# Performance work log

Measured on AMD Instinct MI355X. Metric: run time of the kernel, lower is better.

Reference implementation:

```python
import jax, jax.numpy as jnp
import numpy as np

ALPHA = 0.2  # LeakyReLU negative slope (pyGAT default)
NEG_INF = -9e15


def setup_inputs() -> dict:
    key = jax.random.key(0)
    ks = jax.random.split(key, 8)
    N, IN, OUT, H, C = 4096, 512, 64, 8, 10
    x = jax.random.normal(ks[0], (N, IN), dtype=jnp.float32)
    adj = jax.random.randint(ks[1], (N, N), 0, 2, dtype=jnp.int32)
    W = jax.random.normal(ks[2], (H, IN, OUT), dtype=jnp.float32) * 0.05
    a1 = jax.random.normal(ks[3], (H, OUT), dtype=jnp.float32) * 0.05
    a2 = jax.random.normal(ks[4], (H, OUT), dtype=jnp.float32) * 0.05
    Wo = jax.random.normal(ks[5], (H * OUT, C), dtype=jnp.float32) * 0.05
    ao1 = jax.random.normal(ks[6], (C,), dtype=jnp.float32) * 0.05
    ao2 = jax.random.normal(ks[7], (C,), dtype=jnp.float32) * 0.05
    return {"x": x, "adj": adj, "W": W, "a1": a1, "a2": a2,
            "Wo": Wo, "ao1": ao1, "ao2": ao2}


def _multi_head_gat(h, mask, W, a1, a2):
    # h: [N, F_in], W: [H, F_in, F_out], a1/a2: [H, F_out], mask: [N, N] bool
    Wh = jnp.einsum('ni,hio->hno', h, W)            # [H, N, F_out]
    f1 = jnp.einsum('hno,ho->hn', Wh, a1)           # [H, N]
    f2 = jnp.einsum('hno,ho->hn', Wh, a2)           # [H, N]
    e = f1[:, :, None] + f2[:, None, :]             # [H, N, N]
    e = jnp.where(e > 0, e, ALPHA * e)              # LeakyReLU(0.2)
    e = jnp.where(mask[None, :, :], e, NEG_INF)     # adjacency mask
    attn = jax.nn.softmax(e, axis=-1)               # [H, N, N]
    return jnp.einsum('hnm,hmo->hno', attn, Wh)     # [H, N, F_out]


def reference(x, adj, W, a1, a2, Wo, ao1, ao2):
    mask = adj > 0
    # hidden heads (concat=True -> ELU on concatenated output)
    heads = _multi_head_gat(x, mask, W, a1, a2)          # [H, N, O]
    H, N, O = heads.shape
    hcat = jnp.transpose(heads, (1, 0, 2)).reshape(N, H * O)
    hcat = jax.nn.elu(hcat)
    # output layer (concat=False -> no ELU)
    out = _multi_head_gat(hcat, mask, Wo[None], ao1[None], ao2[None])[0]  # [N, C]
    return jax.nn.log_softmax(out, axis=-1)
```

## Files before the change

### kernel.cpp

```cpp
#include <hip/hip_runtime.h>
#include <hip/hip_bf16.h>
#include <hip/hip_fp16.h>

typedef __bf16 bf16x8 __attribute__((ext_vector_type(8)));
typedef _Float16 h8_t __attribute__((ext_vector_type(8)));
typedef _Float16 v2h __attribute__((ext_vector_type(2)));
typedef short short8 __attribute__((ext_vector_type(8)));
typedef float f32x4 __attribute__((ext_vector_type(4)));

union BF8 { short8 s; bf16x8 b; };
union H8  { short8 s; h8_t h; unsigned w[4]; };
union HU  { _Float16 f; unsigned short u; };

#define N_NODES 4096
#define F_IN 512
#define F_OUT 64
#define NHEAD 8
#define HID 512
#define NCLS 10
#define GAT_ALPHA 0.2f
#define MSPLIT 4
#define WST 4096
#define NWORD (N_NODES / 64)
#define RB 32
#define CB 64
#define NIT ((N_NODES / MSPLIT) / CB)
#define RB2 16
#define MS2 8
#define MT2 (N_NODES / MS2 / 64)

#if defined(__has_builtin)
#if __has_builtin(__builtin_amdgcn_fdot2)
#define FDOT2(a, b, c) __builtin_amdgcn_fdot2((a), (b), (c), false)
#endif
#endif
#ifndef FDOT2
#define FDOT2(a, b, c) ((c) + (float)(a)[0] * (float)(b)[0] + (float)(a)[1] * (float)(b)[1])
#endif

__device__ inline unsigned short f2bf(float f) {
  unsigned u = __builtin_bit_cast(unsigned, f);
  unsigned r = (u + 0x7FFFu + ((u >> 16) & 1u)) >> 16;
  return (unsigned short)r;
}
__device__ inline float bf2f(unsigned short h) {
  unsigned u = ((unsigned)h) << 16;
  return __builtin_bit_cast(float, u);
}

__global__ __launch_bounds__(256) void pack_adj_kernel(
    const int* __restrict__ adj, unsigned long long* __restrict__ bits) {
  int wid = blockIdx.x * 4 + (threadIdx.x >> 6);
  int l = threadIdx.x & 63;
  unsigned long long m = __ballot(adj[(size_t)wid * 64 + l] != 0);
  if (l == 0) bits[wid] = m;
}

__global__ __launch_bounds__(256) void gemm1_kernel(
    const float* __restrict__ x, const float* __restrict__ W,
    const float* __restrict__ a1, const float* __restrict__ a2,
    unsigned short* __restrict__ WhbT, float* __restrict__ rho1,
    unsigned short* __restrict__ E2f16, unsigned short* __restrict__ E2sf16) {
  __shared__ short As[64 * 40];
  __shared__ short Bs[64 * 40];
  __shared__ short Ts[64 * 72];
  const int bx = blockIdx.x;
  const int h  = blockIdx.y;
  const int t  = threadIdx.x;
  const int w  = t >> 6, l = t & 63;
  const int lr = l & 15, ls = l >> 4;
  f32x4 acc[4] = {};
  for (int k0 = 0; k0 < F_IN; k0 += 32) {
    {
      int r = t >> 2, c0 = (t & 3) * 8;
      const float* src = x + (bx * 64 + r) * F_IN + k0 + c0;
      float4 v0 = *(const float4*)src;
      float4 v1 = *(const float4*)(src + 4);
      short8 sv;
      sv[0]=f2bf(v0.x); sv[1]=f2bf(v0.y); sv[2]=f2bf(v0.z); sv[3]=f2bf(v0.w);
      sv[4]=f2bf(v1.x); sv[5]=f2bf(v1.y); sv[6]=f2bf(v1.z); sv[7]=f2bf(v1.w);
      *(short8*)&As[r * 40 + c0] = sv;
    }
    {
      int kk = t >> 3, o0 = (t & 7) * 8;
      const float* src = W + ((h * F_IN) + k0 + kk) * F_OUT + o0;
      float4 v0 = *(const float4*)src;
      float4 v1 = *(const float4*)(src + 4);
      float vv[8] = {v0.x, v0.y, v0.z, v0.w, v1.x, v1.y, v1.z, v1.w};
      #pragma unroll
      for (int i = 0; i < 8; ++i) Bs[(o0 + i) * 40 + kk] = f2bf(vv[i]);
    }
    __syncthreads();
    BF8 a; a.s = *(short8*)&As[(w * 16 + lr) * 40 + ls * 8];
    #pragma unroll
    for (int fc = 0; fc < 4; ++fc) {
      BF8 b; b.s = *(short8*)&Bs[(fc * 16 + lr) * 40 + ls * 8];
      acc[fc] = __builtin_amdgcn_mfma_f32_16x16x32_bf16(a.b, b.b, acc[fc], 0, 0, 0);
    }
    __syncthreads();
  }
  #pragma unroll
  for (int fc = 0; fc < 4; ++fc)
    #pragma unroll
    for (int j = 0; j < 4; ++j) {
      HU hu; hu.f = (_Float16)acc[fc][j];
      Ts[(fc * 16 + lr) * 72 + (w * 16 + ls * 4 + j)] = (short)hu.u;
    }
  __syncthreads();
  {
    int col = t >> 2, seg = t & 3;
    short8 o0 = *(short8*)&Ts[col * 72 + seg * 16];
    short8 o1 = *(short8*)&Ts[col * 72 + seg * 16 + 8];
    unsigned short* dst = WhbT + (size_t)(h * F_OUT + col) * WST + bx * 64 + seg * 16;
    *(short8*)dst = o0;
    *(short8*)(dst + 8) = o1;
  }
  float a1c[4], a2c[4];
  #pragma unroll
  for (int fc = 0; fc < 4; ++fc) {
    a1c[fc] = a1[h * F_OUT + fc * 16 + lr];
    a2c[fc] = a2[h * F_OUT + fc * 16 + lr];
  }
  #pragma unroll
  for (int j = 0; j < 4; ++j) {
    float s1 = 0.f, s2 = 0.f;
    #pragma unroll
    for (int fc = 0; fc < 4; ++fc) { s1 += acc[fc][j] * a1c[fc]; s2 += acc[fc][j] * a2c[fc]; }
    #pragma unroll
    for (int off = 1; off <= 8; off <<= 1) {
      s1 += __shfl_xor(s1, off, 64);
      s2 += __shfl_xor(s2, off, 64);
    }
    if (lr == 0) {
      int row = bx * 64 + w * 16 + ls * 4 + j;
      int idx = h * N_NODES + row;
      rho1[idx] = __expf((GAT_ALPHA - 1.f) * s1);
      HU u1; u1.f = (_Float16)__expf(s2);
      HU u2; u2.f = (_Float16)__expf(GAT_ALPHA * s2);
      E2f16[idx]  = u1.u;
      E2sf16[idx] = u2.u;
    }
  }
}

__global__ __launch_bounds__(512, 4) void att1_kernel(
    const unsigned long long* __restrict__ adjbits,
    const float* __restrict__ rho1,
    const unsigned short* __restrict__ E2f16, const unsigned short* __restrict__ E2sf16,
    const unsigned short* __restrict__ WhbT,
    float* __restrict__ accP, float* __restrict__ SP) {
  __shared__ __align__(16) short Bt[NHEAD][64 * CB];
  const int nb = blockIdx.x * RB;
  const int q  = blockIdx.y;
  const int t  = threadIdx.x;
  const int h  = t >> 6;
  const int l  = t & 63;
  const int r  = l & 15, s = l >> 4;

  const float rho0  = rho1[h * N_NODES + nb + r];
  const float rho1v = rho1[h * N_NODES + nb + 16 + r];
  const v2h rh0 = {(_Float16)rho0, (_Float16)rho0};
  const v2h rh1 = {(_Float16)rho1v, (_Float16)rho1v};
  const v2h ones = {(_Float16)1.0f, (_Float16)1.0f};
  const unsigned short* __restrict__ E2h  = E2f16  + h * N_NODES;
  const unsigned short* __restrict__ E2sh = E2sf16 + h * N_NODES;
  const unsigned long long* __restrict__ ab0 = adjbits + (size_t)(nb + r) * NWORD;
  const unsigned long long* __restrict__ ab1 = adjbits + (size_t)(nb + 16 + r) * NWORD;

  const unsigned short* gsrc0 =
      WhbT + (size_t)(h * F_OUT + (l >> 3)) * WST + (((l & 7) ^ (l >> 3)) * 8);

  const int tb0 = q * (N_NODES / MSPLIT);

  #pragma unroll
  for (int i = 0; i < 8; ++i)
    __builtin_amdgcn_global_load_lds(
        (const __attribute__((address_space(1))) void*)(gsrc0 + tb0 + (size_t)(i * 8) * WST),
        (__attribute__((address_space(3))) void*)&Bt[h][i * 512], 16, 0, 0);

  float S0 = 0.f, S1 = 0.f;
  f32x4 acc[2][4] = {};
  for (int it = 0; it < NIT; ++it) {
    const int tb = tb0 + it * CB;
    const unsigned long long mk0 = ab0[tb >> 6];
    const unsigned long long mk1 = ab1[tb >> 6];
    H8 a0[2], a1f[2];
    #pragma unroll
    for (int kf = 0; kf < 2; ++kf) {
      const int cb = tb + kf * 32 + s * 8;
      uint4 ew = *(const uint4*)(E2h + cb);
      uint4 sw = *(const uint4*)(E2sh + cb);
      const unsigned ewa[4] = {ew.x, ew.y, ew.z, ew.w};
      const unsigned swa[4] = {sw.x, sw.y, sw.z, sw.w};
      const unsigned bm0 = (unsigned)(mk0 >> (kf * 32 + s * 8)) & 0xffu;
      const unsigned bm1 = (unsigned)(mk1 >> (kf * 32 + s * 8)) & 0xffu;
      #pragma unroll
      for (int p = 0; p < 4; ++p) {
        const v2h e2 = __builtin_bit_cast(v2h, ewa[p]);
        const v2h es = __builtin_bit_cast(v2h, swa[p]);
        const unsigned lo0 = ((bm0 >> (2 * p)) & 1u) ? 0x0000FFFFu : 0u;
        const unsigned hi0 = ((bm0 >> (2 * p + 1)) & 1u) ? 0xFFFF0000u : 0u;
        unsigned q0w = __builtin_bit_cast(unsigned, __builtin_elementwise_max(e2, (v2h)(rh0 * es))) & (lo0 | hi0);
        S0 = FDOT2(__builtin_bit_cast(v2h, q0w), ones, S0);
        a0[kf].w[p] = q0w;
        const unsigned lo1 = ((bm1 >> (2 * p)) & 1u) ? 0x0000FFFFu : 0u;
        const unsigned hi1 = ((bm1 >> (2 * p + 1)) & 1u) ? 0xFFFF0000u : 0u;
        unsigned q1w = __builtin_bit_cast(unsigned, __builtin_elementwise_max(e2, (v2h)(rh1 * es))) & (lo1 | hi1);
        S1 = FDOT2(__builtin_bit_cast(v2h, q1w), ones, S1);
        a1f[kf].w[p] = q1w;
      }
    }
    asm volatile("s_waitcnt vmcnt(0)" ::: "memory");
    H8 b[2][4];
    #pragma unroll
    for (int kf = 0; kf < 2; ++kf)
      #pragma unroll
      for (int fc = 0; fc < 4; ++fc)
        b[kf][fc].s = *(short8*)&Bt[h][(fc * 16 + r) * CB + ((kf * 32 + s * 8) ^ ((r & 7) * 8))];
    asm volatile("s_waitcnt lgkmcnt(0)" ::: "memory");
    __builtin_amdgcn_sched_barrier(0);
    if (it + 1 < NIT) {
      #pragma unroll
      for (int i = 0; i < 8; ++i)
        __builtin_amdgcn_global_load_lds(
            (const __attribute__((address_space(1))) void*)(gsrc0 + tb + CB + (size_t)(i * 8) * WST),
            (__attribute__((address_space(3))) void*)&Bt[h][i * 512], 16, 0, 0);
    }
    __builtin_amdgcn_sched_barrier(0);
    #pragma unroll
    for (int kf = 0; kf < 2; ++kf)
      #pragma unroll
      for (int fc = 0; fc < 4; ++fc) {
        acc[0][fc] = __builtin_amdgcn_mfma_f32_16x16x32_f16(a0[kf].h,  b[kf][fc].h, acc[0][fc], 0, 0, 0);
        acc[1][fc] = __builtin_amdgcn_mfma_f32_16x16x32_f16(a1f[kf].h, b[kf][fc].h, acc[1][fc], 0, 0, 0);
      }
  }

  S0 += __shfl_xor(S0, 16, 64); S0 += __shfl_xor(S0, 32, 64);
  S1 += __shfl_xor(S1, 16, 64); S1 += __shfl_xor(S1, 32, 64);
  if (s == 0) {
    SP[((size_t)q * NHEAD + h) * N_NODES + nb + r]      = S0;
    SP[((size_t)q * NHEAD + h) * N_NODES + nb + 16 + r] = S1;
  }
  #pragma unroll
  for (int rg = 0; rg < 2; ++rg)
    #pragma unroll
    for (int fc = 0; fc < 4; ++fc)
      #pragma unroll
      for (int j = 0; j < 4; ++j) {
        int n = nb + rg * 16 + s * 4 + j;
        int col = h * F_OUT + fc * 16 + r;
        accP[((size_t)q * N_NODES + n) * HID + col] = acc[rg][fc][j];
      }
}

__global__ __launch_bounds__(256) void gemm2_kernel(
    const float* __restrict__ accP, const float* __restrict__ SP,
    const float* __restrict__ Wo,
    const float* __restrict__ ao1, const float* __restrict__ ao2,
    unsigned short* __restrict__ Wh2T, float* __restrict__ rho_o,
    float* __restrict__ Eg2, float* __restrict__ Eg2s) {
  int n = blockIdx.x * 4 + (threadIdx.x >> 6);
  int l = threadIdx.x & 63;
  const int h = l >> 3;
  float Ssum = 0.f;
  #pragma unroll
  for (int q = 0; q < MSPLIT; ++q) Ssum += SP[((size_t)q * NHEAD + h) * N_NODES + n];
  float v[8] = {};
  #pragma unroll
  for (int q = 0; q < MSPLIT; ++q) {
    const float* row = accP + ((size_t)q * N_NODES + n) * HID + l * 8;
    float4 va = *(const float4*)row;
    float4 vb = *(const float4*)(row + 4);
    v[0] += va.x; v[1] += va.y; v[2] += va.z; v[3] += va.w;
    v[4] += vb.x; v[5] += vb.y; v[6] += vb.z; v[7] += vb.w;
  }
  float rs = 1.0f / Ssum;
  float acc[NCLS] = {};
  #pragma unroll
  for (int j = 0; j < 8; ++j) {
    float e = v[j] * rs;
    e = e > 0.f ? e : (__expf(e) - 1.0f);
    float hv = bf2f(f2bf(e));
    const float* wrow = Wo + (l * 8 + j) * NCLS;
    #pragma unroll
    for (int c = 0; c < NCLS; ++c) acc[c] += hv * wrow[c];
  }
  #pragma unroll
  for (int c = 0; c < NCLS; ++c)
    #pragma unroll
    for (int off = 32; off > 0; off >>= 1) acc[c] += __shfl_xor(acc[c], off, 64);
  if (l == 0) {
    float s1 = 0.f, s2 = 0.f;
    #pragma unroll
    for (int c = 0; c < NCLS; ++c) {
      s1 += acc[c] * ao1[c];
      s2 += acc[c] * ao2[c];
    }
    #pragma unroll
    for (int c = 0; c < 16; ++c)
      Wh2T[(size_t)c * N_NODES + n] = (c < NCLS) ? f2bf(acc[c]) : (unsigned short)0;
    rho_o[n] = __expf((GAT_ALPHA - 1.f) * s1);
    Eg2[n]   = __expf(s2);
    Eg2s[n]  = __expf(GAT_ALPHA * s2);
  }
}

__global__ __launch_bounds__(512) void att2_kernel(
    const unsigned long long* __restrict__ adjbits,
    const float* __restrict__ rho_o,
    const float* __restrict__ Eg2, const float* __restrict__ Eg2s,
    const unsigned short* __restrict__ Wh2T, float* __restrict__ out) {
  __shared__ float Lacc[MS2][RB2][16];
  __shared__ float LS[MS2][RB2];
  const int nb = blockIdx.x * RB2;
  const int t  = threadIdx.x;
  const int w  = t >> 6;
  const int l  = t & 63;
  const int r  = l & 15, s = l >> 4;
  const int row = nb + r;
  const float ro = rho_o[row];
  const unsigned long long* __restrict__ ab = adjbits + (size_t)row * NWORD;
  const int tb0 = w * (N_NODES / MS2);

  float S = 0.f;
  f32x4 acc = {};
  for (int it = 0; it < MT2; ++it) {
    const int tb = tb0 + it * 64;
    const unsigned long long mk = ab[tb >> 6];
    BF8 a0[2], b0[2];
    #pragma unroll
    for (int kf = 0; kf < 2; ++kf) {
      const int cb = tb + kf * 32 + s * 8;
      b0[kf].s = *(const short8*)(Wh2T + (size_t)r * N_NODES + cb);
      float4 ea = *(const float4*)(Eg2 + cb);
      float4 eb = *(const float4*)(Eg2 + cb + 4);
      float4 sa = *(const float4*)(Eg2s + cb);
      float4 sb = *(const float4*)(Eg2s + cb + 4);
      float ev[8] = {ea.x, ea.y, ea.z, ea.w, eb.x, eb.y, eb.z, eb.w};
      float sv[8] = {sa.x, sa.y, sa.z, sa.w, sb.x, sb.y, sb.z, sb.w};
      const unsigned bm = (unsigned)(mk >> (kf * 32 + s * 8)) & 0xffu;
      #pragma unroll
      for (int j = 0; j < 8; ++j) {
        float qv = fmaxf(ev[j], ro * sv[j]);
        qv = ((bm >> j) & 1u) ? qv : 0.f;
        S += qv;
        a0[kf].b[j] = (__bf16)qv;
      }
    }
    #pragma unroll
    for (int kf = 0; kf < 2; ++kf)
      acc = __builtin_amdgcn_mfma_f32_16x16x32_bf16(a0[kf].b, b0[kf].b, acc, 0, 0, 0);
  }
  S += __shfl_xor(S, 16, 64);
  S += __shfl_xor(S, 32, 64);
  if (s == 0) LS[w][r] = S;
  #pragma unroll
  for (int j = 0; j < 4; ++j) Lacc[w][s * 4 + j][r] = acc[j];
  __syncthreads();
  if (t < 256) {
    const int rr = t >> 4, cc = t & 15;
    float Ssum = 0.f, vsum = 0.f;
    #pragma unroll
    for (int q = 0; q < MS2; ++q) { Ssum += LS[q][rr]; vsum += Lacc[q][rr][cc]; }
    float lo = vsum / Ssum;
    float lom = (cc < NCLS) ? lo : -1e30f;
    float mx = lom;
    #pragma unroll
    for (int off = 1; off <= 8; off <<= 1) mx = fmaxf(mx, __shfl_xor(mx, off, 64));
    float ex = (cc < NCLS) ? __expf(lo - mx) : 0.f;
    float se = ex;
    #pragma unroll
    for (int off = 1; off <= 8; off <<= 1) se += __shfl_xor(se, off, 64);
    float lse = mx + __logf(se);
    if (cc < NCLS) out[(size_t)(nb + rr) * NCLS + cc] = lo - lse;
  }
}

extern "C" void kernel_launch(void* const* d_in, const int* in_sizes, int n_in,
                              void* d_out, int out_size, void* d_ws, size_t ws_size,
                              hipStream_t stream) {
  (void)in_sizes; (void)n_in; (void)out_size; (void)ws_size;
  const float* x   = (const float*)d_in[0];
  const int*   adj = (const int*)d_in[1];
  const float* W   = (const float*)d_in[2];
  const float* a1  = (const float*)d_in[3];
  const float* a2  = (const float*)d_in[4];
  const float* Wo  = (const float*)d_in[5];
  const float* ao1 = (const float*)d_in[6];
  const float* ao2 = (const float*)d_in[7];
  float* out = (float*)d_out;

  char* ws = (char*)d_ws;
  unsigned long long* adjbits = (unsigned long long*)ws; ws += (size_t)N_NODES * NWORD * 8;
  unsigned short* WhbT= (unsigned short*)ws; ws += (size_t)HID * WST * 2;
  float* accP         = (float*)ws;          ws += (size_t)MSPLIT * N_NODES * HID * 4;
  float* SP           = (float*)ws;          ws += (size_t)MSPLIT * NHEAD * N_NODES * 4;
  float* rho1         = (float*)ws;          ws += (size_t)NHEAD * N_NODES * 4;
  unsigned short* E2f16  = (unsigned short*)ws; ws += (size_t)NHEAD * N_NODES * 2;
  unsigned short* E2sf16 = (unsigned short*)ws; ws += (size_t)NHEAD * N_NODES * 2;
  unsigned short* Wh2T= (unsigned short*)ws; ws += (size_t)16 * N_NODES * 2;
  float* rho_o        = (float*)ws;          ws += (size_t)N_NODES * 4;
  float* Eg2          = (float*)ws;          ws += (size_t)N_NODES * 4;
  float* Eg2s         = (float*)ws;          ws += (size_t)N_NODES * 4;

  pack_adj_kernel<<<N_NODES * NWORD / 4, 256, 0, stream>>>(adj, adjbits);
  gemm1_kernel<<<dim3(64, 8), 256, 0, stream>>>(x, W, a1, a2, WhbT, rho1, E2f16, E2sf16);
  att1_kernel<<<dim3(N_NODES / RB, MSPLIT), 512, 0, stream>>>(adjbits, rho1, E2f16, E2sf16, WhbT, accP, SP);
  gemm2_kernel<<<N_NODES / 4, 256, 0, stream>>>(accP, SP, Wo, ao1, ao2, Wh2T, rho_o, Eg2, Eg2s);
  att2_kernel<<<N_NODES / RB2, 512, 0, stream>>>(adjbits, rho_o, Eg2, Eg2s, Wh2T, out);
}
```

Baseline: 119.5 us.

## Pre-convert x and W to bf16 in pack kernel; gemm1 uses direct global-to-LDS loads

The bf16 conversion of x and the transpose-and-convert of W move out of gemm1 and into the adjacency-packing kernel, which writes bf16 copies to workspace. gemm1 then streams these operands straight into LDS with global_load_lds, double-issuing the next k-slice's load before running the MFMAs. This is meant to cut gemm1's per-tile convert and scatter work and to overlap loads with compute. The cost is an extra bf16 round trip through global memory and more work in the first kernel.

```diff
diff --git a/kernel.cpp b/kernel.cpp
--- a/kernel.cpp
+++ b/kernel.cpp
@@ -29,6 +29,10 @@
 #define MS2 8
 #define MT2 (N_NODES / MS2 / 64)
 
+#define PACK_BLOCKS (N_NODES * NWORD / 4)
+#define XCVT_BLOCKS (N_NODES * F_IN / 8 / 256)
+#define WCVT_BLOCKS (NHEAD * F_OUT * F_IN / 8 / 256)
+
 #if defined(__has_builtin)
 #if __has_builtin(__builtin_amdgcn_fdot2)
 #define FDOT2(a, b, c) __builtin_amdgcn_fdot2((a), (b), (c), false)
@@ -48,56 +52,85 @@
   return __builtin_bit_cast(float, u);
 }
 
-__global__ __launch_bounds__(256) void pack_adj_kernel(
-    const int* __restrict__ adj, unsigned long long* __restrict__ bits) {
-  int wid = blockIdx.x * 4 + (threadIdx.x >> 6);
-  int l = threadIdx.x & 63;
-  unsigned long long m = __ballot(adj[(size_t)wid * 64 + l] != 0);
-  if (l == 0) bits[wid] = m;
+__global__ __launch_bounds__(256) void pack_prep_kernel(
+    const int* __restrict__ adj, unsigned long long* __restrict__ bits,
+    const float* __restrict__ x, unsigned short* __restrict__ xbf,
+    const float* __restrict__ W, unsigned short* __restrict__ Wt) {
+  const int b = blockIdx.x;
+  const int tid = threadIdx.x;
+  if (b < PACK_BLOCKS) {
+    int wid = b * 4 + (tid >> 6);
+    int l = tid & 63;
+    unsigned long long m = __ballot(adj[(size_t)wid * 64 + l] != 0);
+    if (l == 0) bits[wid] = m;
+  } else if (b < PACK_BLOCKS + XCVT_BLOCKS) {
+    int idx = (b - PACK_BLOCKS) * 256 + tid;
+    const float* src = x + (size_t)idx * 8;
+    float4 v0 = *(const float4*)src;
+    float4 v1 = *(const float4*)(src + 4);
+    short8 sv;
+    sv[0]=f2bf(v0.x); sv[1]=f2bf(v0.y); sv[2]=f2bf(v0.z); sv[3]=f2bf(v0.w);
+    sv[4]=f2bf(v1.x); sv[5]=f2bf(v1.y); sv[6]=f2bf(v1.z); sv[7]=f2bf(v1.w);
+    *(short8*)&xbf[(size_t)idx * 8] = sv;
+  } else {
+    int t2 = (b - PACK_BLOCKS - XCVT_BLOCKS) * 256 + tid;
+    int h   = t2 >> 12;
+    int rem = t2 & 4095;
+    int o   = rem >> 6;
+    int k8  = rem & 63;
+    const float* src = W + ((size_t)(h * F_IN) + k8 * 8) * F_OUT + o;
+    short8 sv;
+    #pragma unroll
+    for (int j = 0; j < 8; ++j) sv[j] = (short)f2bf(src[(size_t)j * F_OUT]);
+    *(short8*)&Wt[((size_t)(h * F_OUT) + o) * F_IN + k8 * 8] = sv;
+  }
 }
 
 __global__ __launch_bounds__(256) void gemm1_kernel(
-    const float* __restrict__ x, const float* __restrict__ W,
+    const unsigned short* __restrict__ xbf, const unsigned short* __restrict__ Wt,
     const float* __restrict__ a1, const float* __restrict__ a2,
     unsigned short* __restrict__ WhbT, float* __restrict__ rho1,
     unsigned short* __restrict__ E2f16, unsigned short* __restrict__ E2sf16) {
-  __shared__ short As[64 * 40];
-  __shared__ short Bs[64 * 40];
+  __shared__ __align__(16) short As[4 * 512];
+  __shared__ __align__(16) short Bs[4 * 512];
   __shared__ short Ts[64 * 72];
   const int bx = blockIdx.x;
   const int h  = blockIdx.y;
   const int t  = threadIdx.x;
   const int w  = t >> 6, l = t & 63;
   const int lr = l & 15, ls = l >> 4;
+  const unsigned short* asrc = xbf + (size_t)(bx * 64 + w * 16 + lr) * F_IN + ls * 8;
+  const unsigned short* bsrc = Wt + (size_t)(h * F_OUT + w * 16 + lr) * F_IN + ls * 8;
   f32x4 acc[4] = {};
-  for (int k0 = 0; k0 < F_IN; k0 += 32) {
-    {
-      int r = t >> 2, c0 = (t & 3) * 8;
-      const float* src = x + (bx * 64 + r) * F_IN + k0 + c0;
-      float4 v0 = *(const float4*)src;
-      float4 v1 = *(const float4*)(src + 4);
-      short8 sv;
-      sv[0]=f2bf(v0.x); sv[1]=f2bf(v0.y); sv[2]=f2bf(v0.z); sv[3]=f2bf(v0.w);
-      sv[4]=f2bf(v1.x); sv[5]=f2bf(v1.y); sv[6]=f2bf(v1.z); sv[7]=f2bf(v1.w);
-      *(short8*)&As[r * 40 + c0] = sv;
-    }
-    {
-      int kk = t >> 3, o0 = (t & 7) * 8;
-      const float* src = W + ((h * F_IN) + k0 + kk) * F_OUT + o0;
-      float4 v0 = *(const float4*)src;
-      float4 v1 = *(const float4*)(src + 4);
-      float vv[8] = {v0.x, v0.y, v0.z, v0.w, v1.x, v1.y, v1.z, v1.w};
-      #pragma unroll
-      for (int i = 0; i < 8; ++i) Bs[(o0 + i) * 40 + kk] = f2bf(vv[i]);
-    }
+  __builtin_amdgcn_global_load_lds(
+      (const __attribute__((address_space(1))) void*)asrc,
+      (__attribute__((address_space(3))) void*)&As[w * 512], 16, 0, 0);
+  __builtin_amdgcn_global_load_lds(
+      (const __attribute__((address_space(1))) void*)bsrc,
+      (__attribute__((address_space(3))) void*)&Bs[w * 512], 16, 0, 0);
+  for (int it = 0; it < F_IN / 32; ++it) {
+    asm volatile("s_waitcnt vmcnt(0)" ::: "memory");
     __syncthreads();
-    BF8 a; a.s = *(short8*)&As[(w * 16 + lr) * 40 + ls * 8];
-    #pragma unroll
-    for (int fc = 0; fc < 4; ++fc) {
-      BF8 b; b.s = *(short8*)&Bs[(fc * 16 + lr) * 40 + ls * 8];
-      acc[fc] = __builtin_amdgcn_mfma_f32_16x16x32_bf16(a.b, b.b, acc[fc], 0, 0, 0);
-    }
+    BF8 a, b0, b1, b2, b3;
+    a.s  = *(short8*)&As[w * 512 + l * 8];
+    b0.s = *(short8*)&Bs[0 * 512 + l * 8];
+    b1.s = *(short8*)&Bs[1 * 512 + l * 8];
+    b2.s = *(short8*)&Bs[2 * 512 + l * 8];
+    b3.s = *(short8*)&Bs[3 * 512 + l * 8];
+    asm volatile("s_waitcnt lgkmcnt(0)" ::: "memory");
     __syncthreads();
+    if (it + 1 < F_IN / 32) {
+      __builtin_amdgcn_global_load_lds(
+          (const __attribute__((address_space(1))) void*)(asrc + (it + 1) * 32),
+          (__attribute__((address_space(3))) void*)&As[w * 512], 16, 0, 0);
+      __builtin_amdgcn_global_load_lds(
+          (const __attribute__((address_space(1))) void*)(bsrc + (it + 1) * 32),
+          (__attribute__((address_space(3))) void*)&Bs[w * 512], 16, 0, 0);
+    }
+    acc[0] = __builtin_amdgcn_mfma_f32_16x16x32_bf16(a.b, b0.b, acc[0], 0, 0, 0);
+    acc[1] = __builtin_amdgcn_mfma_f32_16x16x32_bf16(a.b, b1.b, acc[1], 0, 0, 0);
+    acc[2] = __builtin_amdgcn_mfma_f32_16x16x32_bf16(a.b, b2.b, acc[2], 0, 0, 0);
+    acc[3] = __builtin_amdgcn_mfma_f32_16x16x32_bf16(a.b, b3.b, acc[3], 0, 0, 0);
   }
   #pragma unroll
   for (int fc = 0; fc < 4; ++fc)
@@ -403,9 +436,12 @@
   float* rho_o        = (float*)ws;          ws += (size_t)N_NODES * 4;
   float* Eg2          = (float*)ws;          ws += (size_t)N_NODES * 4;
   float* Eg2s         = (float*)ws;          ws += (size_t)N_NODES * 4;
-
-  pack_adj_kernel<<<N_NODES * NWORD / 4, 256, 0, stream>>>(adj, adjbits);
-  gemm1_kernel<<<dim3(64, 8), 256, 0, stream>>>(x, W, a1, a2, WhbT, rho1, E2f16, E2sf16);
+  unsigned short* xbf = (unsigned short*)ws; ws += (size_t)N_NODES * F_IN * 2;
+  unsigned short* Wt  = (unsigned short*)ws; ws += (size_t)NHEAD * F_OUT * F_IN * 2;
+
+  pack_prep_kernel<<<PACK_BLOCKS + XCVT_BLOCKS + WCVT_BLOCKS, 256, 0, stream>>>(
+      adj, adjbits, x, xbf, W, Wt);
+  gemm1_kernel<<<dim3(64, 8), 256, 0, stream>>>(xbf, Wt, a1, a2, WhbT, rho1, E2f16, E2sf16);
   att1_kernel<<<dim3(N_NODES / RB, MSPLIT), 512, 0, stream>>>(adjbits, rho1, E2f16, E2sf16, WhbT, accP, SP);
   gemm2_kernel<<<N_NODES / 4, 256, 0, stream>>>(accP, SP, Wo, ao1, ao2, Wh2T, rho_o, Eg2, Eg2s);
   att2_kernel<<<N_NODES / RB2, 512, 0, stream>>>(adjbits, rho_o, Eg2, Eg2s, Wh2T, out);
```

Measured after the change: 113.0 us. 1.06x faster.
